# Kernel optimization log

Measured on AMD Instinct MI355X. Metric: run time of the kernel, lower is better.

The kernel has to match this reference:

```python
import jax, jax.numpy as jnp
import numpy as np

DT = 1e-3   # time step [s] (geometry.dt)
H = 10.0    # grid spacing [m] (geometry.h)

# Staggered-grid first differences (2nd-order accurate on the staggered grid).
# Periodic wrap at the boundary via roll; the damping layer d absorbs there.

def _dplus(f, ax):
    return (jnp.roll(f, -1, axis=ax) - f) / H

def _dminus(f, ax):
    return (f - jnp.roll(f, 1, axis=ax)) / H


def setup_inputs() -> dict:
    key = jax.random.key(0)
    ks = jax.random.split(key, 9)
    B, NZ, NX = 4, 2048, 2048
    vp = 1500.0 + 2500.0 * jax.random.uniform(ks[0], (NZ, NX), jnp.float32)   # P velocity [m/s]
    vs = vp / 1.73                                                            # S velocity (Poisson solid)
    rho = 1000.0 + 1000.0 * jax.random.uniform(ks[1], (NZ, NX), jnp.float32)  # density [kg/m^3]
    fields = {}
    for i, name in enumerate(['vx', 'vz', 'txx', 'tzz', 'txz']):
        fields[name] = 1e-3 * jax.random.normal(ks[2 + i], (B, NZ, NX), jnp.float32)
    d = 50.0 * jax.random.uniform(ks[8], (NZ, NX), jnp.float32)               # PML damping profile
    return dict(vp=vp, vs=vs, rho=rho, **fields, d=d)


def reference(vp, vs, rho, vx, vz, txx, tzz, txz, d):
    # Lame parameters from (vp, vs, rho)
    mu = rho * vs * vs
    lam = rho * vp * vp - 2.0 * mu
    # Split-free damping update: y = (1-c)/(1+c) * y_old + dt/(1+c) * rhs
    c = 0.5 * DT * d            # [nz, nx], broadcasts over shot dim
    a = (1.0 - c) / (1.0 + c)
    b = DT / (1.0 + c)
    # --- velocity update (leapfrog: uses old stresses) ---
    vx_new = a * vx + b * (_dminus(txx, -1) + _dminus(txz, -2)) / rho
    vz_new = a * vz + b * (_dplus(txz, -1) + _dplus(tzz, -2)) / rho
    # --- stress update (uses new velocities) ---
    vx_x = _dplus(vx_new, -1)
    vz_z = _dminus(vz_new, -2)
    txx_new = a * txx + b * ((lam + 2.0 * mu) * vx_x + lam * vz_z)
    tzz_new = a * tzz + b * ((lam + 2.0 * mu) * vz_z + lam * vx_x)
    txz_new = a * txz + b * mu * (_dplus(vx_new, -2) + _dminus(vz_new, -1))
    # hidden state for next time step: [5, B, nz, nx]
    return jnp.stack([vx_new, vz_new, txx_new, tzz_new, txz_new])
```

## Files before the change

### kernel.cpp

```cpp
#include <hip/hip_runtime.h>


constexpr int NZ = 2048;
constexpr int NX = 2048;
constexpr int B  = 4;
constexpr int PLANE = NZ * NX;
constexpr int VOL   = B * PLANE;
constexpr float DT    = 1e-3f;
constexpr float INV_H = 0.1f;

constexpr int ZB = 16;
constexpr int XR = 64;
constexpr int NROW = ZB + 2;
constexpr int RST  = 100;
constexpr int NBLK = PLANE / (ZB * XR);
constexpr int NXCD = 8;
constexpr int BLK_PER_XCD = NBLK / NXCD;

typedef float f32x4 __attribute__((ext_vector_type(4)));

__device__ __forceinline__ float rcpf(float x) { return __builtin_amdgcn_rcpf(x); }
__device__ __forceinline__ float4 ld4(const float* __restrict__ p) {
    return *reinterpret_cast<const float4*>(p);
}
__device__ __forceinline__ void st4(float* __restrict__ p,
                                    float a, float b, float c, float d) {
    f32x4 v = {a, b, c, d};
    *reinterpret_cast<f32x4*>(p) = v;
}

__global__ __launch_bounds__(256) void wave_fused_v10(
    const float* __restrict__ vp,  const float* __restrict__ vs,
    const float* __restrict__ rho,
    const float* __restrict__ vx,  const float* __restrict__ vz,
    const float* __restrict__ txx, const float* __restrict__ tzz,
    const float* __restrict__ txz,
    const float* __restrict__ dd,
    float* __restrict__ out)
{
    __shared__ float lds[5 * NROW * RST];

    const int bid = blockIdx.x;
    const int sb  = (bid & (NXCD - 1)) * BLK_PER_XCD + (bid >> 3);
    const int tz  = sb >> 5;
    const int tx  = sb & 31;
    const int z0  = tz << 4;
    const int x0  = tx << 6;
    const int tid = threadIdx.x;
    const int xt  = tid & 15;
    const int zt  = tid >> 4;

    const int z   = z0 + zt;
    const int x   = x0 + (xt << 2);
    const int zp  = (z + 1) & (NZ - 1);
    const int zm  = (z - 1) & (NZ - 1);
    const int xm1 = (x - 1) & (NX - 1);
    const int xp4 = (x + 4) & (NX - 1);
    const int rz  = z  * NX;
    const int rzp = zp * NX;
    const int rzm = zm * NX;

    float dz6[6], rz6[6];
    {
        const float4 d4 = ld4(dd + rz + x);
        dz6[0] = dd[rz + xm1]; dz6[1] = d4.x; dz6[2] = d4.y;
        dz6[3] = d4.z;         dz6[4] = d4.w; dz6[5] = dd[rz + xp4];
        const float4 r4 = ld4(rho + rz + x);
        rz6[0] = rho[rz + xm1]; rz6[1] = r4.x; rz6[2] = r4.y;
        rz6[3] = r4.z;          rz6[4] = r4.w; rz6[5] = rho[rz + xp4];
    }
    float avz[6], bvz[6], inv_c[4];
    #pragma unroll
    for (int j = 0; j < 6; ++j) {
        const float c   = 0.5f * DT * dz6[j];
        const float inv = rcpf(1.0f + c);
        avz[j] = (1.0f - c) * inv;
        bvz[j] = DT * INV_H * inv * rcpf(rz6[j]);
        if (j >= 1 && j <= 4) inv_c[j - 1] = inv;
    }
    float avzp[4], bvzp[4], avzm[4], bvzm[4];
    {
        const float4 dp = ld4(dd + rzp + x), dm = ld4(dd + rzm + x);
        const float4 rp = ld4(rho + rzp + x), rm = ld4(rho + rzm + x);
        const float dpa[4] = {dp.x, dp.y, dp.z, dp.w};
        const float dma[4] = {dm.x, dm.y, dm.z, dm.w};
        const float rpa[4] = {rp.x, rp.y, rp.z, rp.w};
        const float rma[4] = {rm.x, rm.y, rm.z, rm.w};
        #pragma unroll
        for (int k = 0; k < 4; ++k) {
            float c = 0.5f * DT * dpa[k];
            float inv = rcpf(1.0f + c);
            avzp[k] = (1.0f - c) * inv;
            bvzp[k] = DT * INV_H * inv * rcpf(rpa[k]);
            c = 0.5f * DT * dma[k];
            inv = rcpf(1.0f + c);
            avzm[k] = (1.0f - c) * inv;
            bvzm[k] = DT * INV_H * inv * rcpf(rma[k]);
        }
    }
    float q1[4], q2[4], q3[4];
    {
        const float4 vp4 = ld4(vp + rz + x), vs4 = ld4(vs + rz + x);
        const float vpa[4] = {vp4.x, vp4.y, vp4.z, vp4.w};
        const float vsa[4] = {vs4.x, vs4.y, vs4.z, vs4.w};
        #pragma unroll
        for (int k = 0; k < 4; ++k) {
            const float r   = rz6[k + 1];
            const float muv = r * vsa[k] * vsa[k];
            const float lam = r * vpa[k] * vpa[k] - 2.0f * muv;
            const float bsH = DT * INV_H * inv_c[k];
            q1[k] = bsH * (lam + 2.0f * muv);
            q2[k] = bsH * lam;
            q3[k] = bsH * muv;
        }
    }

    const int lx = 16 + (xt << 2);
    const int rT = (0 * NROW + zt) * RST;
    const int rX = (1 * NROW + zt) * RST;
    const int rZ = (2 * NROW + zt) * RST;
    const int rV = (3 * NROW + zt) * RST;
    const int rW = (4 * NROW + zt) * RST;

    #pragma unroll 1
    for (int b = 0; b < B; ++b) {
        const int b3 = b * PLANE;

        if (b) __syncthreads();

        {
            const float* const ap0 = txx + b3;
            const float* const ap1 = txz + b3;
            const float* const ap2 = tzz + b3;
            const float* const ap3 = vx  + b3;
            const float* const ap4 = vz  + b3;
            #pragma unroll
            for (int a = 0; a < 5; ++a) {
                const float* const ap = (a == 0) ? ap0 : (a == 1) ? ap1
                                      : (a == 2) ? ap2 : (a == 3) ? ap3 : ap4;
                #pragma unroll
                for (int k = 0; k < 2; ++k) {
                    const int idx = k * 256 + tid;
                    if (idx < NROW * 24) {
                        const int r  = idx / 24;
                        const int c  = idx % 24;
                        const int gz = (z0 - 1 + r) & (NZ - 1);
                        const int gx = (x0 - 16 + (c << 2)) & (NX - 1);
                        const f32x4 v =
                            *reinterpret_cast<const f32x4*>(ap + gz * NX + gx);
                        *reinterpret_cast<f32x4*>(
                            &lds[(a * NROW + r) * RST + (c << 2)]) = v;
                    }
                }
            }
        }
        __syncthreads();

        auto L4 = [&](int off) -> f32x4 {
            return *reinterpret_cast<const f32x4*>(&lds[off]);
        };
        float txxz[6], txzz[6], tzzz[5], tzzzp[5], txxzp[5];
        float txzzm[5], vxz[5], vzz[5];
        float txzzp[4], tzzzm[4], vxzp[4], vzzm[4];
        {
            f32x4 m;
            m = L4(rT + RST + lx);
            txxz[1] = m.x; txxz[2] = m.y; txxz[3] = m.z; txxz[4] = m.w;
            txxz[0] = lds[rT + RST + lx - 1];
            txxz[5] = lds[rT + RST + lx + 4];
            m = L4(rX + RST + lx);
            txzz[1] = m.x; txzz[2] = m.y; txzz[3] = m.z; txzz[4] = m.w;
            txzz[0] = lds[rX + RST + lx - 1];
            txzz[5] = lds[rX + RST + lx + 4];
            m = L4(rZ + RST + lx);
            tzzz[1] = m.x; tzzz[2] = m.y; tzzz[3] = m.z; tzzz[4] = m.w;
            tzzz[0] = lds[rZ + RST + lx - 1];
            m = L4(rZ + 2 * RST + lx);
            tzzzp[1] = m.x; tzzzp[2] = m.y; tzzzp[3] = m.z; tzzzp[4] = m.w;
            tzzzp[0] = lds[rZ + 2 * RST + lx - 1];
            m = L4(rT + 2 * RST + lx);
            txxzp[1] = m.x; txxzp[2] = m.y; txxzp[3] = m.z; txxzp[4] = m.w;
            txxzp[0] = lds[rT + 2 * RST + lx - 1];
            m = L4(rX + lx);
            txzzm[0] = m.x; txzzm[1] = m.y; txzzm[2] = m.z; txzzm[3] = m.w;
            txzzm[4] = lds[rX + lx + 4];
            m = L4(rV + RST + lx);
            vxz[0] = m.x; vxz[1] = m.y; vxz[2] = m.z; vxz[3] = m.w;
            vxz[4] = lds[rV + RST + lx + 4];
            m = L4(rW + RST + lx);
            vzz[1] = m.x; vzz[2] = m.y; vzz[3] = m.z; vzz[4] = m.w;
            vzz[0] = lds[rW + RST + lx - 1];
            m = L4(rX + 2 * RST + lx);
            txzzp[0] = m.x; txzzp[1] = m.y; txzzp[2] = m.z; txzzp[3] = m.w;
            m = L4(rZ + lx);
            tzzzm[0] = m.x; tzzzm[1] = m.y; tzzzm[2] = m.z; tzzzm[3] = m.w;
            m = L4(rV + 2 * RST + lx);
            vxzp[0] = m.x; vxzp[1] = m.y; vxzp[2] = m.z; vxzp[3] = m.w;
            m = L4(rW + lx);
            vzzm[0] = m.x; vzzm[1] = m.y; vzzm[2] = m.z; vzzm[3] = m.w;
        }

        float vxn_z[5];
        #pragma unroll
        for (int k = 0; k < 5; ++k)
            vxn_z[k] = avz[k + 1] * vxz[k]
                     + bvz[k + 1] * ((txxz[k + 1] - txxz[k])
                                   + (txzz[k + 1] - txzzm[k]));
        float vzn_z[5];
        #pragma unroll
        for (int k = 0; k < 5; ++k)
            vzn_z[k] = avz[k] * vzz[k]
                     + bvz[k] * ((txzz[k + 1] - txzz[k])
                               + (tzzzp[k] - tzzz[k]));
        float vxn_zp[4];
        #pragma unroll
        for (int k = 0; k < 4; ++k)
            vxn_zp[k] = avzp[k] * vxzp[k]
                      + bvzp[k] * ((txxzp[k + 1] - txxzp[k])
                                 + (txzzp[k] - txzz[k + 1]));
        float vzn_zm[4];
        #pragma unroll
        for (int k = 0; k < 4; ++k)
            vzn_zm[k] = avzm[k] * vzzm[k]
                      + bvzm[k] * ((txzzm[k + 1] - txzzm[k])
                                 + (tzzz[k + 1] - tzzzm[k]));

        float oxx[4], ozz[4], oxz[4];
        #pragma unroll
        for (int k = 0; k < 4; ++k) {
            const float dvx = vxn_z[k + 1] - vxn_z[k];
            const float dvz = vzn_z[k + 1] - vzn_zm[k];
            oxx[k] = avz[k + 1] * txxz[k + 1] + q1[k] * dvx + q2[k] * dvz;
            ozz[k] = avz[k + 1] * tzzz[k + 1] + q1[k] * dvz + q2[k] * dvx;
            oxz[k] = avz[k + 1] * txzz[k + 1]
                   + q3[k] * ((vxn_zp[k] - vxn_z[k])
                            + (vzn_z[k + 1] - vzn_z[k]));
        }

        const int cz = b3 + rz + x;
        st4(out + 0 * VOL + cz, vxn_z[0], vxn_z[1], vxn_z[2], vxn_z[3]);
        st4(out + 1 * VOL + cz, vzn_z[1], vzn_z[2], vzn_z[3], vzn_z[4]);
        st4(out + 2 * VOL + cz, oxx[0], oxx[1], oxx[2], oxx[3]);
        st4(out + 3 * VOL + cz, ozz[0], ozz[1], ozz[2], ozz[3]);
        st4(out + 4 * VOL + cz, oxz[0], oxz[1], oxz[2], oxz[3]);
    }
}

extern "C" void kernel_launch(void* const* d_in, const int* in_sizes, int n_in,
                              void* d_out, int out_size, void* d_ws, size_t ws_size,
                              hipStream_t stream) {
    const float* vp  = (const float*)d_in[0];
    const float* vs  = (const float*)d_in[1];
    const float* rho = (const float*)d_in[2];
    const float* vx  = (const float*)d_in[3];
    const float* vz  = (const float*)d_in[4];
    const float* txx = (const float*)d_in[5];
    const float* tzz = (const float*)d_in[6];
    const float* txz = (const float*)d_in[7];
    const float* dd  = (const float*)d_in[8];
    float* out = (float*)d_out;

    const int threads = 256;
    const int blocks  = NBLK;
    hipLaunchKernelGGL(wave_fused_v10, dim3(blocks), dim3(threads), 0, stream,
                       vp, vs, rho, vx, vz, txx, tzz, txz, dd, out);
}
```

Measured before the change: 647.7 us.

## Reshape stencil tile to 8x128 with narrow halo and flattened staging loads

Changes the block tile from 16x64 to 8x128 and shrinks the x halo from 16 floats to 4 per side. The per-thread staging addresses for the five fields are precomputed once and loaded as seven float4s per shot instead of a guarded nested loop. Scalar halo reads from LDS become aligned float4 reads. The aim is to cut redundant halo traffic and index arithmetic. The trade-off is a larger relative z-halo (10 rows for 8 output rows) and more registers held for the precomputed pointers.

```diff
diff --git a/kernel.cpp b/kernel.cpp
--- a/kernel.cpp
+++ b/kernel.cpp
@@ -9,10 +9,13 @@
 constexpr float DT    = 1e-3f;
 constexpr float INV_H = 0.1f;
 
-constexpr int ZB = 16;
-constexpr int XR = 64;
+constexpr int ZB   = 8;
+constexpr int XR   = 128;
 constexpr int NROW = ZB + 2;
-constexpr int RST  = 100;
+constexpr int RF4  = 34;
+constexpr int ROWF = 140;
+constexpr int F4PF = NROW * RF4;
+constexpr int TOT  = 5 * F4PF;
 constexpr int NBLK = PLANE / (ZB * XR);
 constexpr int NXCD = 8;
 constexpr int BLK_PER_XCD = NBLK / NXCD;
@@ -29,7 +32,7 @@
     *reinterpret_cast<f32x4*>(p) = v;
 }
 
-__global__ __launch_bounds__(256) void wave_fused_v10(
+__global__ __launch_bounds__(256) void wave_fused_v12(
     const float* __restrict__ vp,  const float* __restrict__ vs,
     const float* __restrict__ rho,
     const float* __restrict__ vx,  const float* __restrict__ vz,
@@ -38,17 +41,17 @@
     const float* __restrict__ dd,
     float* __restrict__ out)
 {
-    __shared__ float lds[5 * NROW * RST];
+    __shared__ float lds[5 * NROW * ROWF];
 
     const int bid = blockIdx.x;
     const int sb  = (bid & (NXCD - 1)) * BLK_PER_XCD + (bid >> 3);
-    const int tz  = sb >> 5;
-    const int tx  = sb & 31;
-    const int z0  = tz << 4;
-    const int x0  = tx << 6;
+    const int tz  = sb >> 4;
+    const int tx  = sb & 15;
+    const int z0  = tz << 3;
+    const int x0  = tx << 7;
     const int tid = threadIdx.x;
-    const int xt  = tid & 15;
-    const int zt  = tid >> 4;
+    const int xt  = tid & 31;
+    const int zt  = tid >> 5;
 
     const int z   = z0 + zt;
     const int x   = x0 + (xt << 2);
@@ -60,6 +63,27 @@
     const int rzp = zp * NX;
     const int rzm = zm * NX;
 
+    const float* sp[7];
+    int dst7[7];
+    {
+        #pragma unroll
+        for (int k = 0; k < 7; ++k) {
+            const int idx = k * 256 + tid;
+            const int f   = idx / F4PF;
+            const int rem = idx - f * F4PF;
+            const int rr  = rem / RF4;
+            const int c   = rem - rr * RF4;
+            const int gz  = (z0 - 1 + rr) & (NZ - 1);
+            const int gx  = (x0 - 4 + (c << 2)) & (NX - 1);
+            const float* fp = (f == 0) ? txx : (f == 1) ? txz
+                            : (f == 2) ? tzz : (f == 3) ? vx
+                            : (f == 4) ? vz  : txx;
+            sp[k]   = fp + gz * NX + gx;
+            dst7[k] = (f * NROW + rr) * ROWF + (c << 2);
+        }
+    }
+    const bool act6 = tid < (TOT - 6 * 256);
+
     float dz6[6], rz6[6];
     {
         const float4 d4 = ld4(dd + rz + x);
@@ -115,12 +139,15 @@
         }
     }
 
-    const int lx = 16 + (xt << 2);
-    const int rT = (0 * NROW + zt) * RST;
-    const int rX = (1 * NROW + zt) * RST;
-    const int rZ = (2 * NROW + zt) * RST;
-    const int rV = (3 * NROW + zt) * RST;
-    const int rW = (4 * NROW + zt) * RST;
+    const int lx   = 4 + (xt << 2);
+    const int rowT = (0 * NROW + zt) * ROWF + lx;
+    const int rowX = (1 * NROW + zt) * ROWF + lx;
+    const int rowZ = (2 * NROW + zt) * ROWF + lx;
+    const int rowV = (3 * NROW + zt) * ROWF + lx;
+    const int rowW = (4 * NROW + zt) * ROWF + lx;
+    auto L4 = [&](int off) -> f32x4 {
+        return *reinterpret_cast<const f32x4*>(&lds[off]);
+    };
 
     #pragma unroll 1
     for (int b = 0; b < B; ++b) {
@@ -128,76 +155,56 @@
 
         if (b) __syncthreads();
 
-        {
-            const float* const ap0 = txx + b3;
-            const float* const ap1 = txz + b3;
-            const float* const ap2 = tzz + b3;
-            const float* const ap3 = vx  + b3;
-            const float* const ap4 = vz  + b3;
-            #pragma unroll
-            for (int a = 0; a < 5; ++a) {
-                const float* const ap = (a == 0) ? ap0 : (a == 1) ? ap1
-                                      : (a == 2) ? ap2 : (a == 3) ? ap3 : ap4;
-                #pragma unroll
-                for (int k = 0; k < 2; ++k) {
-                    const int idx = k * 256 + tid;
-                    if (idx < NROW * 24) {
-                        const int r  = idx / 24;
-                        const int c  = idx % 24;
-                        const int gz = (z0 - 1 + r) & (NZ - 1);
-                        const int gx = (x0 - 16 + (c << 2)) & (NX - 1);
-                        const f32x4 v =
-                            *reinterpret_cast<const f32x4*>(ap + gz * NX + gx);
-                        *reinterpret_cast<f32x4*>(
-                            &lds[(a * NROW + r) * RST + (c << 2)]) = v;
-                    }
-                }
-            }
-        }
+        f32x4 sv[7];
+        #pragma unroll
+        for (int k = 0; k < 7; ++k)
+            sv[k] = *reinterpret_cast<const f32x4*>(sp[k] + b3);
+        #pragma unroll
+        for (int k = 0; k < 6; ++k)
+            *reinterpret_cast<f32x4*>(&lds[dst7[k]]) = sv[k];
+        if (act6)
+            *reinterpret_cast<f32x4*>(&lds[dst7[6]]) = sv[6];
         __syncthreads();
 
-        auto L4 = [&](int off) -> f32x4 {
-            return *reinterpret_cast<const f32x4*>(&lds[off]);
-        };
         float txxz[6], txzz[6], tzzz[5], tzzzp[5], txxzp[5];
         float txzzm[5], vxz[5], vzz[5];
-        float txzzp[4], tzzzm[4], vxzp[4], vzzm[4];
+        float txzzp4[4], tzzzm4[4], vxzp4[4], vzzm4[4];
         {
-            f32x4 m;
-            m = L4(rT + RST + lx);
+            f32x4 m, e;
+            m = L4(rowT + ROWF);      e = L4(rowT + ROWF - 4);
             txxz[1] = m.x; txxz[2] = m.y; txxz[3] = m.z; txxz[4] = m.w;
-            txxz[0] = lds[rT + RST + lx - 1];
-            txxz[5] = lds[rT + RST + lx + 4];
-            m = L4(rX + RST + lx);
+            txxz[0] = e.w;            e = L4(rowT + ROWF + 4);
+            txxz[5] = e.x;
+            m = L4(rowX + ROWF);      e = L4(rowX + ROWF - 4);
             txzz[1] = m.x; txzz[2] = m.y; txzz[3] = m.z; txzz[4] = m.w;
-            txzz[0] = lds[rX + RST + lx - 1];
-            txzz[5] = lds[rX + RST + lx + 4];
-            m = L4(rZ + RST + lx);
+            txzz[0] = e.w;            e = L4(rowX + ROWF + 4);
+            txzz[5] = e.x;
+            m = L4(rowZ + ROWF);      e = L4(rowZ + ROWF - 4);
             tzzz[1] = m.x; tzzz[2] = m.y; tzzz[3] = m.z; tzzz[4] = m.w;
-            tzzz[0] = lds[rZ + RST + lx - 1];
-            m = L4(rZ + 2 * RST + lx);
+            tzzz[0] = e.w;
+            m = L4(rowZ + 2 * ROWF);  e = L4(rowZ + 2 * ROWF - 4);
             tzzzp[1] = m.x; tzzzp[2] = m.y; tzzzp[3] = m.z; tzzzp[4] = m.w;
-            tzzzp[0] = lds[rZ + 2 * RST + lx - 1];
-            m = L4(rT + 2 * RST + lx);
+            tzzzp[0] = e.w;
+            m = L4(rowT + 2 * ROWF);  e = L4(rowT + 2 * ROWF - 4);
             txxzp[1] = m.x; txxzp[2] = m.y; txxzp[3] = m.z; txxzp[4] = m.w;
-            txxzp[0] = lds[rT + 2 * RST + lx - 1];
-            m = L4(rX + lx);
+            txxzp[0] = e.w;
+            m = L4(rowX);             e = L4(rowX + 4);
             txzzm[0] = m.x; txzzm[1] = m.y; txzzm[2] = m.z; txzzm[3] = m.w;
-            txzzm[4] = lds[rX + lx + 4];
-            m = L4(rV + RST + lx);
+            txzzm[4] = e.x;
+            m = L4(rowV + ROWF);      e = L4(rowV + ROWF + 4);
             vxz[0] = m.x; vxz[1] = m.y; vxz[2] = m.z; vxz[3] = m.w;
-            vxz[4] = lds[rV + RST + lx + 4];
-            m = L4(rW + RST + lx);
+            vxz[4] = e.x;
+            m = L4(rowW + ROWF);      e = L4(rowW + ROWF - 4);
             vzz[1] = m.x; vzz[2] = m.y; vzz[3] = m.z; vzz[4] = m.w;
-            vzz[0] = lds[rW + RST + lx - 1];
-            m = L4(rX + 2 * RST + lx);
-            txzzp[0] = m.x; txzzp[1] = m.y; txzzp[2] = m.z; txzzp[3] = m.w;
-            m = L4(rZ + lx);
-            tzzzm[0] = m.x; tzzzm[1] = m.y; tzzzm[2] = m.z; tzzzm[3] = m.w;
-            m = L4(rV + 2 * RST + lx);
-            vxzp[0] = m.x; vxzp[1] = m.y; vxzp[2] = m.z; vxzp[3] = m.w;
-            m = L4(rW + lx);
-            vzzm[0] = m.x; vzzm[1] = m.y; vzzm[2] = m.z; vzzm[3] = m.w;
+            vzz[0] = e.w;
+            m = L4(rowX + 2 * ROWF);
+            txzzp4[0] = m.x; txzzp4[1] = m.y; txzzp4[2] = m.z; txzzp4[3] = m.w;
+            m = L4(rowZ);
+            tzzzm4[0] = m.x; tzzzm4[1] = m.y; tzzzm4[2] = m.z; tzzzm4[3] = m.w;
+            m = L4(rowV + 2 * ROWF);
+            vxzp4[0] = m.x; vxzp4[1] = m.y; vxzp4[2] = m.z; vxzp4[3] = m.w;
+            m = L4(rowW);
+            vzzm4[0] = m.x; vzzm4[1] = m.y; vzzm4[2] = m.z; vzzm4[3] = m.w;
         }
 
         float vxn_z[5];
@@ -215,15 +222,15 @@
         float vxn_zp[4];
         #pragma unroll
         for (int k = 0; k < 4; ++k)
-            vxn_zp[k] = avzp[k] * vxzp[k]
+            vxn_zp[k] = avzp[k] * vxzp4[k]
                       + bvzp[k] * ((txxzp[k + 1] - txxzp[k])
-                                 + (txzzp[k] - txzz[k + 1]));
+                                 + (txzzp4[k] - txzz[k + 1]));
         float vzn_zm[4];
         #pragma unroll
         for (int k = 0; k < 4; ++k)
-            vzn_zm[k] = avzm[k] * vzzm[k]
+            vzn_zm[k] = avzm[k] * vzzm4[k]
                       + bvzm[k] * ((txzzm[k + 1] - txzzm[k])
-                                 + (tzzz[k + 1] - tzzzm[k]));
+                                 + (tzzz[k + 1] - tzzzm4[k]));
 
         float oxx[4], ozz[4], oxz[4];
         #pragma unroll
@@ -262,6 +269,6 @@
 
     const int threads = 256;
     const int blocks  = NBLK;
-    hipLaunchKernelGGL(wave_fused_v10, dim3(blocks), dim3(threads), 0, stream,
+    hipLaunchKernelGGL(wave_fused_v12, dim3(blocks), dim3(threads), 0, stream,
                        vp, vs, rho, vx, vz, txx, tzz, txz, dd, out);
 }
```

Result: faster. 597.1 us (-7.8%).
